# Kernel optimization log

Measured on AMD Instinct MI355X. Metric: run time of the kernel, lower is better.

## Reference

```python
import jax, jax.numpy as jnp
import numpy as np

N_SRC, N_DST, E = 32768, 8192, 65536
NODE_IN, EDGE_IN, HIDDEN = 64, 32, 64


def setup_inputs() -> dict:
    key = jax.random.key(0)
    ks = jax.random.split(key, 8)
    node_features = jax.random.normal(ks[0], (N_SRC, NODE_IN), dtype=jnp.float32)
    edge_features = jax.random.normal(ks[1], (E, EDGE_IN), dtype=jnp.float32)
    src_idx = jax.random.randint(ks[2], (E,), 0, N_SRC, dtype=jnp.int32)
    dst_idx = jax.random.randint(ks[3], (E,), 0, N_DST, dtype=jnp.int32)
    # edge_layer: Linear(edge_in, hidden*node_in); node_layer: Linear(node_in+hidden, hidden)
    s_e = 1.0 / np.sqrt(EDGE_IN)
    s_n = 1.0 / np.sqrt(NODE_IN + HIDDEN)
    W_e = jax.random.uniform(ks[4], (EDGE_IN, HIDDEN * NODE_IN), jnp.float32, -s_e, s_e)
    b_e = jax.random.uniform(ks[5], (HIDDEN * NODE_IN,), jnp.float32, -s_e, s_e)
    W_n = jax.random.uniform(ks[6], (NODE_IN + HIDDEN, HIDDEN), jnp.float32, -s_n, s_n)
    b_n = jax.random.uniform(ks[7], (HIDDEN,), jnp.float32, -s_n, s_n)
    return {"node_features": node_features, "edge_features": edge_features,
            "src_idx": src_idx, "dst_idx": dst_idx,
            "W_e": W_e, "b_e": b_e, "W_n": W_n, "b_n": b_n, "n_dst": N_DST}


def reference(node_features, edge_features, src_idx, dst_idx, W_e, b_e, W_n, b_n, n_dst):
    # Dropout is identity in eval mode.
    # Edge-conditioned weight generation: [E, hidden*node_in] -> [E, hidden, node_in]
    ew = jax.nn.relu(edge_features @ W_e + b_e).reshape(-1, HIDDEN, NODE_IN)
    h_src = node_features[src_idx]                       # [E, node_in] gather
    m = jnp.einsum('ehd,ed->eh', ew, h_src)              # per-edge matvec -> [E, hidden]
    # segment mean over destination nodes (mailbox mean)
    msum = jax.ops.segment_sum(m, dst_idx, num_segments=n_dst)
    cnt = jax.ops.segment_sum(jnp.ones((m.shape[0],), m.dtype), dst_idx, num_segments=n_dst)
    h_neigh = jnp.where(cnt[:, None] > 0, msum / jnp.maximum(cnt[:, None], 1.0), 0.0)
    h_self = node_features[:n_dst]
    h = jnp.concatenate([h_self, h_neigh], axis=1)       # [n_dst, node_in+hidden]
    return jax.nn.relu(h @ W_n + b_n)
```

## Files before the change

kernel.cpp:

```cpp
#include <hip/hip_runtime.h>


typedef float f32x4 __attribute__((ext_vector_type(4)));
typedef float f32x2 __attribute__((ext_vector_type(2)));
typedef __bf16 bf16x8 __attribute__((ext_vector_type(8)));
typedef __bf16 bf16x4 __attribute__((ext_vector_type(4)));

#define E_TOT   65536
#define NDST    8192
#define EPW     72
#define EPF     68

__global__ __launch_bounds__(256) void prep_kernel(
    const float* __restrict__ We, const float* __restrict__ be,
    __bf16* __restrict__ Wp, float* __restrict__ bp) {
  int tid = blockIdx.x * 256 + threadIdx.x;
  int T = tid >> 6, l = tid & 63;
  int d0 = T >> 2, ht = T & 3;
  int c = l & 15, kg = l >> 4;
  int ncol = (ht * 16 + c) * 64 + d0;
  bf16x8 v;
#pragma unroll
  for (int j = 0; j < 8; ++j) v[j] = (__bf16)We[(kg * 8 + j) * 4096 + ncol];
  *reinterpret_cast<bf16x8*>(Wp + tid * 8) = v;
  if (l < 16) bp[T * 16 + l] = be[(ht * 16 + l) * 64 + d0];
}

__global__ __launch_bounds__(256) void scan_kernel(const int* __restrict__ cnt_i,
                                                   int* __restrict__ off,
                                                   int* __restrict__ cursor) {
  __shared__ int wsum[4];
  const int t = threadIdx.x;
  const int lane = t & 63, w = t >> 6;
  int vals[32];
  const int4* cp = (const int4*)(cnt_i + t * 32);
#pragma unroll
  for (int i = 0; i < 8; ++i) {
    int4 v = cp[i];
    vals[i * 4 + 0] = v.x; vals[i * 4 + 1] = v.y;
    vals[i * 4 + 2] = v.z; vals[i * 4 + 3] = v.w;
  }
  int loc[32];
  int s = 0;
#pragma unroll
  for (int i = 0; i < 32; ++i) { loc[i] = s; s += vals[i]; }
  int inc = s;
#pragma unroll
  for (int d = 1; d < 64; d <<= 1) {
    int n = __shfl_up(inc, d, 64);
    if (lane >= d) inc += n;
  }
  if (lane == 63) wsum[w] = inc;
  __syncthreads();
  int base = inc - s;
#pragma unroll
  for (int i = 0; i < 4; ++i)
    if (i < w) base += wsum[i];
#pragma unroll
  for (int i = 0; i < 32; ++i) {
    int v = base + loc[i];
    off[t * 32 + i] = v;
    cursor[t * 32 + i] = v;
  }
  if (t == 255) off[8192] = E_TOT;
}

__global__ void fill_kernel(const int* __restrict__ dst, int* __restrict__ cursor,
                            int* __restrict__ eid) {
  int e = blockIdx.x * 256 + threadIdx.x;
  int slot = atomicAdd(&cursor[dst[e]], 1);
  eid[slot] = e;
}

__global__ __launch_bounds__(256, 2) void edge5_kernel(
    const float* __restrict__ nf, const float* __restrict__ ef,
    const int* __restrict__ src, const int* __restrict__ dst,
    const __bf16* __restrict__ Wp, const float* __restrict__ bp,
    float* __restrict__ m, int* __restrict__ cnt_i) {
  __shared__ float hs[64 * EPF];
  const int t = threadIdx.x;
  const int eblk = blockIdx.x << 6;

  {
    const int el = t & 63, q = t >> 6;
    const int srow = src[eblk + el];
    const f32x4* nfr = (const f32x4*)(nf + (srow << 6) + (q << 4));
#pragma unroll
    for (int i = 0; i < 4; ++i) {
      f32x4 v = nfr[i];
      const int dbase = (q << 4) + i * 4;
      hs[(dbase + 0) * EPF + el] = v[0];
      hs[(dbase + 1) * EPF + el] = v[1];
      hs[(dbase + 2) * EPF + el] = v[2];
      hs[(dbase + 3) * EPF + el] = v[3];
    }
  }

  if (t < 64) atomicAdd(&cnt_i[dst[eblk + t]], 1);

  const int w = t >> 6, l = t & 63;
  const int c = l & 15, g = l >> 4;

  bf16x8 afr[4];
#pragma unroll
  for (int as = 0; as < 4; ++as) {
    const int e = eblk + as * 16 + c;
    const f32x4* p = (const f32x4*)(ef + (e << 5) + (g << 3));
    f32x4 v0 = p[0], v1 = p[1];
    bf16x8 a;
    a[0] = (__bf16)v0[0]; a[1] = (__bf16)v0[1]; a[2] = (__bf16)v0[2]; a[3] = (__bf16)v0[3];
    a[4] = (__bf16)v1[0]; a[5] = (__bf16)v1[1]; a[6] = (__bf16)v1[2]; a[7] = (__bf16)v1[3];
    afr[as] = a;
  }

  __syncthreads();

  f32x2 accA[4], accB[4];
#pragma unroll
  for (int i = 0; i < 4; ++i) {
    accA[i][0] = 0.f; accA[i][1] = 0.f;
    accB[i][0] = 0.f; accB[i][1] = 0.f;
  }

  const bf16x8* WpV = (const bf16x8*)Wp;

  bf16x8 bfrA = WpV[(0 * 4 + w) * 64 + l];
  float  bvA  = bp[(0 * 4 + w) * 16 + c];
  bf16x8 bfrB = WpV[(1 * 4 + w) * 64 + l];
  float  bvB  = bp[(1 * 4 + w) * 16 + c];

#pragma unroll 8
  for (int dl = 0; dl < 64; dl += 2) {
    {
      const bf16x8 bcur = bfrA;
      const f32x4 cb = {bvA, bvA, bvA, bvA};
      if (dl + 2 < 64) {
        bfrA = WpV[((dl + 2) * 4 + w) * 64 + l];
        bvA  = bp[((dl + 2) * 4 + w) * 16 + c];
      }
#pragma unroll
      for (int as = 0; as < 4; ++as) {
        const f32x4 hvf = *(const f32x4*)&hs[dl * EPF + as * 16 + (g << 2)];
        f32x4 tmp = __builtin_amdgcn_mfma_f32_16x16x32_bf16(afr[as], bcur, cb, 0, 0, 0);
        f32x2 tl = {fmaxf(tmp[0], 0.f), fmaxf(tmp[1], 0.f)};
        f32x2 th = {fmaxf(tmp[2], 0.f), fmaxf(tmp[3], 0.f)};
        f32x2 hl = __builtin_shufflevector(hvf, hvf, 0, 1);
        f32x2 hh = __builtin_shufflevector(hvf, hvf, 2, 3);
        asm("v_pk_fma_f32 %0, %1, %2, %0" : "+v"(accA[as]) : "v"(tl), "v"(hl));
        asm("v_pk_fma_f32 %0, %1, %2, %0" : "+v"(accB[as]) : "v"(th), "v"(hh));
      }
    }
    {
      const bf16x8 bcur = bfrB;
      const f32x4 cb = {bvB, bvB, bvB, bvB};
      if (dl + 3 < 64) {
        bfrB = WpV[((dl + 3) * 4 + w) * 64 + l];
        bvB  = bp[((dl + 3) * 4 + w) * 16 + c];
      }
#pragma unroll
      for (int as = 0; as < 4; ++as) {
        const f32x4 hvf = *(const f32x4*)&hs[(dl + 1) * EPF + as * 16 + (g << 2)];
        f32x4 tmp = __builtin_amdgcn_mfma_f32_16x16x32_bf16(afr[as], bcur, cb, 0, 0, 0);
        f32x2 tl = {fmaxf(tmp[0], 0.f), fmaxf(tmp[1], 0.f)};
        f32x2 th = {fmaxf(tmp[2], 0.f), fmaxf(tmp[3], 0.f)};
        f32x2 hl = __builtin_shufflevector(hvf, hvf, 0, 1);
        f32x2 hh = __builtin_shufflevector(hvf, hvf, 2, 3);
        asm("v_pk_fma_f32 %0, %1, %2, %0" : "+v"(accA[as]) : "v"(tl), "v"(hl));
        asm("v_pk_fma_f32 %0, %1, %2, %0" : "+v"(accB[as]) : "v"(th), "v"(hh));
      }
    }
  }

  const int hbase = (w << 4) + c;
#pragma unroll
  for (int as = 0; as < 4; ++as) {
    const int ebase = eblk + as * 16 + (g << 2);
    m[((ebase + 0) << 6) + hbase] = accA[as][0];
    m[((ebase + 1) << 6) + hbase] = accA[as][1];
    m[((ebase + 2) << 6) + hbase] = accB[as][0];
    m[((ebase + 3) << 6) + hbase] = accB[as][1];
  }
}

__global__ __launch_bounds__(256) void final5_kernel(
    const float* __restrict__ nf, const float* __restrict__ m,
    const int* __restrict__ off, const int* __restrict__ eid,
    const float* __restrict__ Wn, const float* __restrict__ bn,
    float* __restrict__ out) {
  __shared__ float wn_s[128 * 64];
  __shared__ float hn_s[8 * 64];
  const int t = threadIdx.x;
#pragma unroll
  for (int i = 0; i < 8; ++i)
    ((f32x4*)wn_s)[i * 256 + t] = ((const f32x4*)Wn)[i * 256 + t];

  const int w = t >> 6, h = t & 63;
  const int row0 = blockIdx.x * 8 + w * 2;

#pragma unroll
  for (int i = 0; i < 2; ++i) {
    const int d = row0 + i;
    const int lo = off[d], hi = off[d + 1];
    float a0 = 0.f, a1 = 0.f;
    int j = lo;
    for (; j + 2 <= hi; j += 2) {
      const int e0 = eid[j], e1 = eid[j + 1];
      a0 += m[(e0 << 6) + h];
      a1 += m[(e1 << 6) + h];
    }
    if (j < hi) a0 += m[(eid[j] << 6) + h];
    const float a = a0 + a1;
    hn_s[(w * 2 + i) * 64 + h] = (hi > lo) ? a * (1.f / (float)(hi - lo)) : 0.f;
  }
  __syncthreads();

  const float bv = bn[h];
  float acc[2] = {bv, bv};
#pragma unroll 4
  for (int k = 0; k < 64; ++k) {
    const float wv = wn_s[k * 64 + h];
#pragma unroll
    for (int i = 0; i < 2; ++i)
      acc[i] = fmaf(nf[(row0 + i) * 64 + k], wv, acc[i]);
  }
#pragma unroll 4
  for (int k = 0; k < 64; ++k) {
    const float wv = wn_s[(64 + k) * 64 + h];
#pragma unroll
    for (int i = 0; i < 2; ++i)
      acc[i] = fmaf(hn_s[(w * 2 + i) * 64 + k], wv, acc[i]);
  }
#pragma unroll
  for (int i = 0; i < 2; ++i)
    out[(row0 + i) * 64 + h] = fmaxf(acc[i], 0.f);
}


__global__ __launch_bounds__(256, 4) void edge_kernel(
    const float* __restrict__ nf, const float* __restrict__ ef,
    const int* __restrict__ src, const int* __restrict__ dst,
    const __bf16* __restrict__ Wp, const float* __restrict__ bp,
    float* __restrict__ msum, float* __restrict__ cnt_g) {
  __shared__ __bf16 hs[64 * EPW];
  const int t = threadIdx.x;
  const int eblk = blockIdx.x << 6;
  {
    const int el = t & 63, q = t >> 6;
    const int srow = src[eblk + el];
    const f32x4* nfr = (const f32x4*)(nf + (srow << 6) + (q << 4));
#pragma unroll
    for (int i = 0; i < 4; ++i) {
      f32x4 v = nfr[i];
      const int dbase = (q << 4) + i * 4;
      hs[(dbase + 0) * EPW + el] = (__bf16)v[0];
      hs[(dbase + 1) * EPW + el] = (__bf16)v[1];
      hs[(dbase + 2) * EPW + el] = (__bf16)v[2];
      hs[(dbase + 3) * EPW + el] = (__bf16)v[3];
    }
  }
  const int w = t >> 6, l = t & 63, c = l & 15, g = l >> 4;
  bf16x8 afr[4];
#pragma unroll
  for (int as = 0; as < 4; ++as) {
    const int e = eblk + as * 16 + c;
    const f32x4* p = (const f32x4*)(ef + (e << 5) + (g << 3));
    f32x4 v0 = p[0], v1 = p[1];
    bf16x8 a;
    a[0] = (__bf16)v0[0]; a[1] = (__bf16)v0[1]; a[2] = (__bf16)v0[2]; a[3] = (__bf16)v0[3];
    a[4] = (__bf16)v1[0]; a[5] = (__bf16)v1[1]; a[6] = (__bf16)v1[2]; a[7] = (__bf16)v1[3];
    afr[as] = a;
  }
  __syncthreads();
  f32x4 acc[4];
#pragma unroll
  for (int i = 0; i < 4; ++i) { acc[i][0]=0.f; acc[i][1]=0.f; acc[i][2]=0.f; acc[i][3]=0.f; }
  const bf16x8* WpV = (const bf16x8*)Wp;
  const f32x4 zero = {0.f, 0.f, 0.f, 0.f};
#pragma unroll 4
  for (int d0 = 0; d0 < 64; ++d0) {
    const int T = d0 * 4 + w;
    const bf16x8 bfr = WpV[T * 64 + l];
    const float bv = bp[T * 16 + c];
    const f32x4 cb = {bv, bv, bv, bv};
#pragma unroll
    for (int as = 0; as < 4; ++as) {
      const bf16x4 hv = *(const bf16x4*)&hs[d0 * EPW + as * 16 + (g << 2)];
      const f32x4 hvf = {(float)hv[0], (float)hv[1], (float)hv[2], (float)hv[3]};
      f32x4 tmp = __builtin_amdgcn_mfma_f32_16x16x32_bf16(afr[as], bfr, cb, 0, 0, 0);
      tmp = __builtin_elementwise_max(tmp, zero);
      acc[as] = tmp * hvf + acc[as];
    }
  }
#pragma unroll
  for (int as = 0; as < 4; ++as)
#pragma unroll
    for (int r = 0; r < 4; ++r) {
      const int e = eblk + as * 16 + (g << 2) + r;
      const int dd = dst[e];
      unsafeAtomicAdd(msum + (dd << 6) + (w << 4) + c, acc[as][r]);
      if (w == 0 && c == 0) unsafeAtomicAdd(cnt_g + dd, 1.0f);
    }
}

__global__ __launch_bounds__(256) void final_kernel(
    const float* __restrict__ nf, const float* __restrict__ msum,
    const float* __restrict__ cnt, const float* __restrict__ Wn,
    const float* __restrict__ bn, float* __restrict__ out) {
  __shared__ float wn_s[128 * 64];
  const int t = threadIdx.x;
#pragma unroll
  for (int i = 0; i < 8; ++i)
    ((f32x4*)wn_s)[i * 256 + t] = ((const f32x4*)Wn)[i * 256 + t];
  __syncthreads();
  const int w = t >> 6, h = t & 63;
  const int row0 = blockIdx.x * 16 + w * 4;
  const float bv = bn[h];
  float acc[4] = {bv, bv, bv, bv};
  float s[4];
#pragma unroll
  for (int i = 0; i < 4; ++i) {
    const float cv = cnt[row0 + i];
    s[i] = cv > 0.f ? 1.f / cv : 0.f;
  }
#pragma unroll 4
  for (int k = 0; k < 64; ++k) {
    const float wv = wn_s[k * 64 + h];
#pragma unroll
    for (int i = 0; i < 4; ++i) acc[i] = fmaf(nf[(row0 + i) * 64 + k], wv, acc[i]);
  }
#pragma unroll 4
  for (int k = 0; k < 64; ++k) {
    const float wv = wn_s[(64 + k) * 64 + h];
#pragma unroll
    for (int i = 0; i < 4; ++i) acc[i] = fmaf(msum[(row0 + i) * 64 + k] * s[i], wv, acc[i]);
  }
#pragma unroll
  for (int i = 0; i < 4; ++i) out[(row0 + i) * 64 + h] = fmaxf(acc[i], 0.f);
}


extern "C" void kernel_launch(void* const* d_in, const int* in_sizes, int n_in,
                              void* d_out, int out_size, void* d_ws, size_t ws_size,
                              hipStream_t stream) {
  const float* nf  = (const float*)d_in[0];
  const float* ef  = (const float*)d_in[1];
  const int*   src = (const int*)d_in[2];
  const int*   dst = (const int*)d_in[3];
  const float* We  = (const float*)d_in[4];
  const float* be  = (const float*)d_in[5];
  const float* Wn  = (const float*)d_in[6];
  const float* bn  = (const float*)d_in[7];
  float* out = (float*)d_out;
  char* ws = (char*)d_ws;

  const size_t MB = 16777216;
  const size_t T_OFF    = MB;
  const size_t T_CURSOR = T_OFF + 36864;
  const size_t T_CNTI   = T_CURSOR + 32768;
  const size_t T_EID    = T_CNTI + 32768;
  const size_t T_WP     = T_EID + 262144;
  const size_t T_BP     = T_WP + 262144;
  const size_t NEED     = T_BP + 16384;

  if (ws_size >= NEED) {
    float*  m      = (float*)ws;
    int*    off    = (int*)(ws + T_OFF);
    int*    cursor = (int*)(ws + T_CURSOR);
    int*    cnt_i  = (int*)(ws + T_CNTI);
    int*    eid    = (int*)(ws + T_EID);
    __bf16* Wp     = (__bf16*)(ws + T_WP);
    float*  bp     = (float*)(ws + T_BP);

    hipMemsetAsync(cnt_i, 0, 32768, stream);
    prep_kernel<<<64, 256, 0, stream>>>(We, be, Wp, bp);
    edge5_kernel<<<E_TOT / 64, 256, 0, stream>>>(nf, ef, src, dst, Wp, bp, m, cnt_i);
    scan_kernel<<<1, 256, 0, stream>>>(cnt_i, off, cursor);
    fill_kernel<<<E_TOT / 256, 256, 0, stream>>>(dst, cursor, eid);
    final5_kernel<<<NDST / 8, 256, 0, stream>>>(nf, m, off, eid, Wn, bn, out);
  } else {
    float* msum = (float*)ws;
    float* cnt  = (float*)(ws + 2097152);
    const size_t need = 2097152 + 32768 + 262144 + 16384;
    __bf16* Wp;
    float*  bp;
    if (ws_size >= need) {
      Wp = (__bf16*)(ws + 2097152 + 32768);
      bp = (float*)(ws + 2097152 + 32768 + 262144);
    } else {
      Wp = (__bf16*)d_out;
      bp = (float*)((char*)d_out + 262144);
    }
    hipMemsetAsync(msum, 0, 2097152 + 32768, stream);
    prep_kernel<<<64, 256, 0, stream>>>(We, be, Wp, bp);
    edge_kernel<<<E_TOT / 64, 256, 0, stream>>>(nf, ef, src, dst, Wp, bp, msum, cnt);
    final_kernel<<<NDST / 16, 256, 0, stream>>>(nf, msum, cnt, Wn, bn, out);
  }
}
```

Measured before the change: 79.74 us.

## Remap edge kernel warps to edge subtiles sharing A fragment across hidden tiles

Each wave now owns 16 edges and loops over all four hidden tiles, instead of owning one hidden tile and looping over all 64 edges. It holds one A fragment (edge features) in registers but loads four B fragments per d step from global/L2, and reads one LDS vector per step instead of four. Launch bounds are raised to 4 blocks per SM to increase occupancy. The cost is four times as many weight-fragment loads per wave per step, and more live B registers under a tighter register budget.

```diff
diff --git a/kernel.cpp b/kernel.cpp
--- a/kernel.cpp
+++ b/kernel.cpp
@@ -72,7 +72,7 @@
   eid[slot] = e;
 }
 
-__global__ __launch_bounds__(256, 2) void edge5_kernel(
+__global__ __launch_bounds__(256, 4) void edge6_kernel(
     const float* __restrict__ nf, const float* __restrict__ ef,
     const int* __restrict__ src, const int* __restrict__ dst,
     const __bf16* __restrict__ Wp, const float* __restrict__ bp,
@@ -101,19 +101,33 @@
   const int w = t >> 6, l = t & 63;
   const int c = l & 15, g = l >> 4;
 
-  bf16x8 afr[4];
-#pragma unroll
-  for (int as = 0; as < 4; ++as) {
-    const int e = eblk + as * 16 + c;
+  bf16x8 afr;
+  {
+    const int e = eblk + (w << 4) + c;
     const f32x4* p = (const f32x4*)(ef + (e << 5) + (g << 3));
     f32x4 v0 = p[0], v1 = p[1];
-    bf16x8 a;
-    a[0] = (__bf16)v0[0]; a[1] = (__bf16)v0[1]; a[2] = (__bf16)v0[2]; a[3] = (__bf16)v0[3];
-    a[4] = (__bf16)v1[0]; a[5] = (__bf16)v1[1]; a[6] = (__bf16)v1[2]; a[7] = (__bf16)v1[3];
-    afr[as] = a;
-  }
-
-  __syncthreads();
+    afr[0] = (__bf16)v0[0]; afr[1] = (__bf16)v0[1]; afr[2] = (__bf16)v0[2]; afr[3] = (__bf16)v0[3];
+    afr[4] = (__bf16)v1[0]; afr[5] = (__bf16)v1[1]; afr[6] = (__bf16)v1[2]; afr[7] = (__bf16)v1[3];
+  }
+
+  const bf16x8* WpV = (const bf16x8*)Wp;
+
+  bf16x8 bA0 = WpV[(0 * 4 + 0) * 64 + l];
+  bf16x8 bA1 = WpV[(0 * 4 + 1) * 64 + l];
+  bf16x8 bA2 = WpV[(0 * 4 + 2) * 64 + l];
+  bf16x8 bA3 = WpV[(0 * 4 + 3) * 64 + l];
+  float  vA0 = bp[(0 * 4 + 0) * 16 + c];
+  float  vA1 = bp[(0 * 4 + 1) * 16 + c];
+  float  vA2 = bp[(0 * 4 + 2) * 16 + c];
+  float  vA3 = bp[(0 * 4 + 3) * 16 + c];
+  bf16x8 bB0 = WpV[(1 * 4 + 0) * 64 + l];
+  bf16x8 bB1 = WpV[(1 * 4 + 1) * 64 + l];
+  bf16x8 bB2 = WpV[(1 * 4 + 2) * 64 + l];
+  bf16x8 bB3 = WpV[(1 * 4 + 3) * 64 + l];
+  float  vB0 = bp[(1 * 4 + 0) * 16 + c];
+  float  vB1 = bp[(1 * 4 + 1) * 16 + c];
+  float  vB2 = bp[(1 * 4 + 2) * 16 + c];
+  float  vB3 = bp[(1 * 4 + 3) * 16 + c];
 
   f32x2 accA[4], accB[4];
 #pragma unroll
@@ -122,63 +136,84 @@
     accB[i][0] = 0.f; accB[i][1] = 0.f;
   }
 
-  const bf16x8* WpV = (const bf16x8*)Wp;
-
-  bf16x8 bfrA = WpV[(0 * 4 + w) * 64 + l];
-  float  bvA  = bp[(0 * 4 + w) * 16 + c];
-  bf16x8 bfrB = WpV[(1 * 4 + w) * 64 + l];
-  float  bvB  = bp[(1 * 4 + w) * 16 + c];
-
-#pragma unroll 8
-  for (int dl = 0; dl < 64; dl += 2) {
+  __syncthreads();
+
+  const int hoff = (w << 4) + (g << 2);
+  f32x4 hvA = *(const f32x4*)&hs[0 * EPF + hoff];
+  f32x4 hvB = *(const f32x4*)&hs[1 * EPF + hoff];
+
+#define EDGE_SECTION(B0, B1, B2, B3, V0, V1, V2, V3, HV)                            \
+  {                                                                                  \
+    const f32x4 cb0 = {V0, V0, V0, V0};                                              \
+    const f32x4 cb1 = {V1, V1, V1, V1};                                              \
+    const f32x4 cb2 = {V2, V2, V2, V2};                                              \
+    const f32x4 cb3 = {V3, V3, V3, V3};                                              \
+    f32x4 t0 = __builtin_amdgcn_mfma_f32_16x16x32_bf16(afr, B0, cb0, 0, 0, 0);       \
+    f32x4 t1 = __builtin_amdgcn_mfma_f32_16x16x32_bf16(afr, B1, cb1, 0, 0, 0);       \
+    f32x4 t2 = __builtin_amdgcn_mfma_f32_16x16x32_bf16(afr, B2, cb2, 0, 0, 0);       \
+    f32x4 t3 = __builtin_amdgcn_mfma_f32_16x16x32_bf16(afr, B3, cb3, 0, 0, 0);       \
+    f32x2 hl = __builtin_shufflevector(HV, HV, 0, 1);                                \
+    f32x2 hh = __builtin_shufflevector(HV, HV, 2, 3);                                \
+    f32x2 p;                                                                         \
+    p[0] = fmaxf(t0[0], 0.f); p[1] = fmaxf(t0[1], 0.f);                              \
+    asm("v_pk_fma_f32 %0, %1, %2, %0" : "+v"(accA[0]) : "v"(p), "v"(hl));            \
+    p[0] = fmaxf(t0[2], 0.f); p[1] = fmaxf(t0[3], 0.f);                              \
+    asm("v_pk_fma_f32 %0, %1, %2, %0" : "+v"(accB[0]) : "v"(p), "v"(hh));            \
+    p[0] = fmaxf(t1[0], 0.f); p[1] = fmaxf(t1[1], 0.f);                              \
+    asm("v_pk_fma_f32 %0, %1, %2, %0" : "+v"(accA[1]) : "v"(p), "v"(hl));            \
+    p[0] = fmaxf(t1[2], 0.f); p[1] = fmaxf(t1[3], 0.f);                              \
+    asm("v_pk_fma_f32 %0, %1, %2, %0" : "+v"(accB[1]) : "v"(p), "v"(hh));            \
+    p[0] = fmaxf(t2[0], 0.f); p[1] = fmaxf(t2[1], 0.f);                              \
+    asm("v_pk_fma_f32 %0, %1, %2, %0" : "+v"(accA[2]) : "v"(p), "v"(hl));            \
+    p[0] = fmaxf(t2[2], 0.f); p[1] = fmaxf(t2[3], 0.f);                              \
+    asm("v_pk_fma_f32 %0, %1, %2, %0" : "+v"(accB[2]) : "v"(p), "v"(hh));            \
+    p[0] = fmaxf(t3[0], 0.f); p[1] = fmaxf(t3[1], 0.f);                              \
+    asm("v_pk_fma_f32 %0, %1, %2, %0" : "+v"(accA[3]) : "v"(p), "v"(hl));            \
+    p[0] = fmaxf(t3[2], 0.f); p[1] = fmaxf(t3[3], 0.f);                              \
+    asm("v_pk_fma_f32 %0, %1, %2, %0" : "+v"(accB[3]) : "v"(p), "v"(hh));            \
+  }
+
+  for (int d0 = 0; d0 < 64; d0 += 2) {
     {
-      const bf16x8 bcur = bfrA;
-      const f32x4 cb = {bvA, bvA, bvA, bvA};
-      if (dl + 2 < 64) {
-        bfrA = WpV[((dl + 2) * 4 + w) * 64 + l];
-        bvA  = bp[((dl + 2) * 4 + w) * 16 + c];
+      const bf16x8 u0 = bA0, u1 = bA1, u2 = bA2, u3 = bA3;
+      const float  x0 = vA0, x1 = vA1, x2 = vA2, x3 = vA3;
+      const f32x4  hv = hvA;
+      if (d0 + 2 < 64) {
+        const int Tn = (d0 + 2) * 4;
+        bA0 = WpV[(Tn + 0) * 64 + l];  vA0 = bp[(Tn + 0) * 16 + c];
+        bA1 = WpV[(Tn + 1) * 64 + l];  vA1 = bp[(Tn + 1) * 16 + c];
+        bA2 = WpV[(Tn + 2) * 64 + l];  vA2 = bp[(Tn + 2) * 16 + c];
+        bA3 = WpV[(Tn + 3) * 64 + l];  vA3 = bp[(Tn + 3) * 16 + c];
+        hvA = *(const f32x4*)&hs[(d0 + 2) * EPF + hoff];
       }
-#pragma unroll
-      for (int as = 0; as < 4; ++as) {
-        const f32x4 hvf = *(const f32x4*)&hs[dl * EPF + as * 16 + (g << 2)];
-        f32x4 tmp = __builtin_amdgcn_mfma_f32_16x16x32_bf16(afr[as], bcur, cb, 0, 0, 0);
-        f32x2 tl = {fmaxf(tmp[0], 0.f), fmaxf(tmp[1], 0.f)};
-        f32x2 th = {fmaxf(tmp[2], 0.f), fmaxf(tmp[3], 0.f)};
-        f32x2 hl = __builtin_shufflevector(hvf, hvf, 0, 1);
-        f32x2 hh = __builtin_shufflevector(hvf, hvf, 2, 3);
-        asm("v_pk_fma_f32 %0, %1, %2, %0" : "+v"(accA[as]) : "v"(tl), "v"(hl));
-        asm("v_pk_fma_f32 %0, %1, %2, %0" : "+v"(accB[as]) : "v"(th), "v"(hh));
+      EDGE_SECTION(u0, u1, u2, u3, x0, x1, x2, x3, hv)
+    }
+    {
+      const bf16x8 u0 = bB0, u1 = bB1, u2 = bB2, u3 = bB3;
+      const float  x0 = vB0, x1 = vB1, x2 = vB2, x3 = vB3;
+      const f32x4  hv = hvB;
+      if (d0 + 3 < 64) {
+        const int Tn = (d0 + 3) * 4;
+        bB0 = WpV[(Tn + 0) * 64 + l];  vB0 = bp[(Tn + 0) * 16 + c];
+        bB1 = WpV[(Tn + 1) * 64 + l];  vB1 = bp[(Tn + 1) * 16 + c];
+        bB2 = WpV[(Tn + 2) * 64 + l];  vB2 = bp[(Tn + 2) * 16 + c];
+        bB3 = WpV[(Tn + 3) * 64 + l];  vB3 = bp[(Tn + 3) * 16 + c];
+        hvB = *(const f32x4*)&hs[(d0 + 3) * EPF + hoff];
       }
-    }
-    {
-      const bf16x8 bcur = bfrB;
-      const f32x4 cb = {bvB, bvB, bvB, bvB};
-      if (dl + 3 < 64) {
-        bfrB = WpV[((dl + 3) * 4 + w) * 64 + l];
-        bvB  = bp[((dl + 3) * 4 + w) * 16 + c];
-      }
-#pragma unroll
-      for (int as = 0; as < 4; ++as) {
-        const f32x4 hvf = *(const f32x4*)&hs[(dl + 1) * EPF + as * 16 + (g << 2)];
-        f32x4 tmp = __builtin_amdgcn_mfma_f32_16x16x32_bf16(afr[as], bcur, cb, 0, 0, 0);
-        f32x2 tl = {fmaxf(tmp[0], 0.f), fmaxf(tmp[1], 0.f)};
-        f32x2 th = {fmaxf(tmp[2], 0.f), fmaxf(tmp[3], 0.f)};
-        f32x2 hl = __builtin_shufflevector(hvf, hvf, 0, 1);
-        f32x2 hh = __builtin_shufflevector(hvf, hvf, 2, 3);
-        asm("v_pk_fma_f32 %0, %1, %2, %0" : "+v"(accA[as]) : "v"(tl), "v"(hl));
-        asm("v_pk_fma_f32 %0, %1, %2, %0" : "+v"(accB[as]) : "v"(th), "v"(hh));
-      }
-    }
-  }
-
-  const int hbase = (w << 4) + c;
-#pragma unroll
-  for (int as = 0; as < 4; ++as) {
-    const int ebase = eblk + as * 16 + (g << 2);
-    m[((ebase + 0) << 6) + hbase] = accA[as][0];
-    m[((ebase + 1) << 6) + hbase] = accA[as][1];
-    m[((ebase + 2) << 6) + hbase] = accB[as][0];
-    m[((ebase + 3) << 6) + hbase] = accB[as][1];
+      EDGE_SECTION(u0, u1, u2, u3, x0, x1, x2, x3, hv)
+    }
+  }
+#undef EDGE_SECTION
+
+  const int ebase = eblk + (w << 4) + (g << 2);
+#pragma unroll
+  for (int ht = 0; ht < 4; ++ht) {
+    const int hcol = (ht << 4) + c;
+    f32x2 a = accA[ht], b = accB[ht];
+    m[((ebase + 0) << 6) + hcol] = a[0];
+    m[((ebase + 1) << 6) + hcol] = a[1];
+    m[((ebase + 2) << 6) + hcol] = b[0];
+    m[((ebase + 3) << 6) + hcol] = b[1];
   }
 }
 
@@ -373,7 +408,7 @@
 
     hipMemsetAsync(cnt_i, 0, 32768, stream);
     prep_kernel<<<64, 256, 0, stream>>>(We, be, Wp, bp);
-    edge5_kernel<<<E_TOT / 64, 256, 0, stream>>>(nf, ef, src, dst, Wp, bp, m, cnt_i);
+    edge6_kernel<<<E_TOT / 64, 256, 0, stream>>>(nf, ef, src, dst, Wp, bp, m, cnt_i);
     scan_kernel<<<1, 256, 0, stream>>>(cnt_i, off, cursor);
     fill_kernel<<<E_TOT / 256, 256, 0, stream>>>(dst, cursor, eid);
     final5_kernel<<<NDST / 8, 256, 0, stream>>>(nf, m, off, eid, Wn, bn, out);
```

After: 117.6 us. 47.5% more time.

## Restructure edge kernel: 128 edges per block, double-buffered LDS weight staging

Applied to the files above, without the earlier changes.

The edge kernel now handles 128 edges per block instead of 64. Each wave owns 32 edges across all 64 hidden columns, and the generated-weight fragments are staged through double-buffered shared memory in 16 windows. This raises reuse of the W_e fragments loaded from global memory and halves the block count. Gathered source-node features are stored in LDS as bf16, which shrinks LDS traffic but adds rounding error. The separate memset of the degree counter is folded into the prep kernel, saving one launch.

```diff
diff --git a/kernel.cpp b/kernel.cpp
--- a/kernel.cpp
+++ b/kernel.cpp
@@ -9,12 +9,13 @@
 #define E_TOT   65536
 #define NDST    8192
 #define EPW     72
-#define EPF     68
+#define EP2     136
 
 __global__ __launch_bounds__(256) void prep_kernel(
     const float* __restrict__ We, const float* __restrict__ be,
-    __bf16* __restrict__ Wp, float* __restrict__ bp) {
+    __bf16* __restrict__ Wp, float* __restrict__ bp, int* __restrict__ cnt_i) {
   int tid = blockIdx.x * 256 + threadIdx.x;
+  if (tid < NDST) cnt_i[tid] = 0;
   int T = tid >> 6, l = tid & 63;
   int d0 = T >> 2, ht = T & 3;
   int c = l & 15, kg = l >> 4;
@@ -72,113 +73,132 @@
   eid[slot] = e;
 }
 
-__global__ __launch_bounds__(256, 2) void edge5_kernel(
+__global__ __launch_bounds__(256, 2) void edge7_kernel(
     const float* __restrict__ nf, const float* __restrict__ ef,
     const int* __restrict__ src, const int* __restrict__ dst,
     const __bf16* __restrict__ Wp, const float* __restrict__ bp,
     float* __restrict__ m, int* __restrict__ cnt_i) {
-  __shared__ float hs[64 * EPF];
+  __shared__ __align__(16) __bf16 hs[64 * EP2];
+  __shared__ uint4 wp_s[2][1024];
+  __shared__ float bias_s[2][256];
   const int t = threadIdx.x;
-  const int eblk = blockIdx.x << 6;
+  const int eblk = blockIdx.x << 7;
 
   {
-    const int el = t & 63, q = t >> 6;
+    const int el = t & 127, q = t >> 7;
     const int srow = src[eblk + el];
-    const f32x4* nfr = (const f32x4*)(nf + (srow << 6) + (q << 4));
-#pragma unroll
-    for (int i = 0; i < 4; ++i) {
+    const f32x4* nfr = (const f32x4*)(nf + (srow << 6) + (q << 5));
+#pragma unroll
+    for (int i = 0; i < 8; ++i) {
       f32x4 v = nfr[i];
-      const int dbase = (q << 4) + i * 4;
-      hs[(dbase + 0) * EPF + el] = v[0];
-      hs[(dbase + 1) * EPF + el] = v[1];
-      hs[(dbase + 2) * EPF + el] = v[2];
-      hs[(dbase + 3) * EPF + el] = v[3];
-    }
-  }
-
-  if (t < 64) atomicAdd(&cnt_i[dst[eblk + t]], 1);
+      const int d = (q << 5) + (i << 2);
+      hs[(d + 0) * EP2 + el] = (__bf16)v[0];
+      hs[(d + 1) * EP2 + el] = (__bf16)v[1];
+      hs[(d + 2) * EP2 + el] = (__bf16)v[2];
+      hs[(d + 3) * EP2 + el] = (__bf16)v[3];
+    }
+  }
+
+  if (t < 128) atomicAdd(&cnt_i[dst[eblk + t]], 1);
 
   const int w = t >> 6, l = t & 63;
   const int c = l & 15, g = l >> 4;
-
-  bf16x8 afr[4];
-#pragma unroll
-  for (int as = 0; as < 4; ++as) {
-    const int e = eblk + as * 16 + c;
-    const f32x4* p = (const f32x4*)(ef + (e << 5) + (g << 3));
-    f32x4 v0 = p[0], v1 = p[1];
-    bf16x8 a;
-    a[0] = (__bf16)v0[0]; a[1] = (__bf16)v0[1]; a[2] = (__bf16)v0[2]; a[3] = (__bf16)v0[3];
-    a[4] = (__bf16)v1[0]; a[5] = (__bf16)v1[1]; a[6] = (__bf16)v1[2]; a[7] = (__bf16)v1[3];
-    afr[as] = a;
+  const uint4* WpQ = (const uint4*)Wp;
+  const int bpos = (((t >> 6) * 16) + (t & 15)) * 4 + ((t >> 4) & 3);
+
+  bf16x8 afrA, afrB;
+  {
+    const int e0 = eblk + (w << 5) + c;
+    const f32x4* p0 = (const f32x4*)(ef + (e0 << 5) + (g << 3));
+    f32x4 v0 = p0[0], v1 = p0[1];
+    afrA[0] = (__bf16)v0[0]; afrA[1] = (__bf16)v0[1]; afrA[2] = (__bf16)v0[2]; afrA[3] = (__bf16)v0[3];
+    afrA[4] = (__bf16)v1[0]; afrA[5] = (__bf16)v1[1]; afrA[6] = (__bf16)v1[2]; afrA[7] = (__bf16)v1[3];
+    const f32x4* p1 = (const f32x4*)(ef + ((e0 + 16) << 5) + (g << 3));
+    f32x4 u0 = p1[0], u1 = p1[1];
+    afrB[0] = (__bf16)u0[0]; afrB[1] = (__bf16)u0[1]; afrB[2] = (__bf16)u0[2]; afrB[3] = (__bf16)u0[3];
+    afrB[4] = (__bf16)u1[0]; afrB[5] = (__bf16)u1[1]; afrB[6] = (__bf16)u1[2]; afrB[7] = (__bf16)u1[3];
+  }
+
+  {
+    uint4 s0 = WpQ[t], s1 = WpQ[256 + t], s2 = WpQ[512 + t], s3 = WpQ[768 + t];
+    float sb = bp[t];
+    wp_s[0][t] = s0; wp_s[0][256 + t] = s1; wp_s[0][512 + t] = s2; wp_s[0][768 + t] = s3;
+    bias_s[0][bpos] = sb;
+  }
+
+  f32x4 accA[4], accB[4];
+#pragma unroll
+  for (int i = 0; i < 4; ++i) {
+    accA[i][0]=0.f; accA[i][1]=0.f; accA[i][2]=0.f; accA[i][3]=0.f;
+    accB[i][0]=0.f; accB[i][1]=0.f; accB[i][2]=0.f; accB[i][3]=0.f;
   }
 
   __syncthreads();
 
-  f32x2 accA[4], accB[4];
-#pragma unroll
-  for (int i = 0; i < 4; ++i) {
-    accA[i][0] = 0.f; accA[i][1] = 0.f;
-    accB[i][0] = 0.f; accB[i][1] = 0.f;
-  }
-
-  const bf16x8* WpV = (const bf16x8*)Wp;
-
-  bf16x8 bfrA = WpV[(0 * 4 + w) * 64 + l];
-  float  bvA  = bp[(0 * 4 + w) * 16 + c];
-  bf16x8 bfrB = WpV[(1 * 4 + w) * 64 + l];
-  float  bvB  = bp[(1 * 4 + w) * 16 + c];
-
-#pragma unroll 8
-  for (int dl = 0; dl < 64; dl += 2) {
-    {
-      const bf16x8 bcur = bfrA;
-      const f32x4 cb = {bvA, bvA, bvA, bvA};
-      if (dl + 2 < 64) {
-        bfrA = WpV[((dl + 2) * 4 + w) * 64 + l];
-        bvA  = bp[((dl + 2) * 4 + w) * 16 + c];
+  const int hoffA = (w << 5) + (g << 2);
+  int cur = 0;
+
+  for (int win = 0; win < 16; ++win) {
+    uint4 s0, s1, s2, s3; float sb;
+    const bool pf = (win < 15);
+    if (pf) {
+      const int base = (win + 1) << 10;
+      s0 = WpQ[base + t]; s1 = WpQ[base + 256 + t];
+      s2 = WpQ[base + 512 + t]; s3 = WpQ[base + 768 + t];
+      sb = bp[((win + 1) << 8) + t];
+    }
+
+    const bf16x8* wpf = (const bf16x8*)&wp_s[cur][0];
+    const float*  bsf = &bias_s[cur][0];
+#pragma unroll
+    for (int dl = 0; dl < 4; ++dl) {
+      const int d0 = (win << 2) + dl;
+      const bf16x8 wf0 = wpf[(dl * 4 + 0) * 64 + l];
+      const bf16x8 wf1 = wpf[(dl * 4 + 1) * 64 + l];
+      const bf16x8 wf2 = wpf[(dl * 4 + 2) * 64 + l];
+      const bf16x8 wf3 = wpf[(dl * 4 + 3) * 64 + l];
+      const f32x4  bv4 = *(const f32x4*)&bsf[(dl * 16 + c) * 4];
+      const bf16x4 hva = *(const bf16x4*)&hs[d0 * EP2 + hoffA];
+      const bf16x4 hvb = *(const bf16x4*)&hs[d0 * EP2 + hoffA + 16];
+      const f32x4 ha = {(float)hva[0], (float)hva[1], (float)hva[2], (float)hva[3]};
+      const f32x4 hb = {(float)hvb[0], (float)hvb[1], (float)hvb[2], (float)hvb[3]};
+      const f32x4 zero = {0.f, 0.f, 0.f, 0.f};
+#define DO_HT(HT, WF)                                                                 \
+      {                                                                               \
+        const f32x4 cb = {bv4[HT], bv4[HT], bv4[HT], bv4[HT]};                        \
+        f32x4 ta = __builtin_amdgcn_mfma_f32_16x16x32_bf16(afrA, WF, cb, 0, 0, 0);    \
+        ta = __builtin_elementwise_max(ta, zero);                                     \
+        accA[HT] = ta * ha + accA[HT];                                                \
+        f32x4 tb = __builtin_amdgcn_mfma_f32_16x16x32_bf16(afrB, WF, cb, 0, 0, 0);    \
+        tb = __builtin_elementwise_max(tb, zero);                                     \
+        accB[HT] = tb * hb + accB[HT];                                                \
       }
-#pragma unroll
-      for (int as = 0; as < 4; ++as) {
-        const f32x4 hvf = *(const f32x4*)&hs[dl * EPF + as * 16 + (g << 2)];
-        f32x4 tmp = __builtin_amdgcn_mfma_f32_16x16x32_bf16(afr[as], bcur, cb, 0, 0, 0);
-        f32x2 tl = {fmaxf(tmp[0], 0.f), fmaxf(tmp[1], 0.f)};
-        f32x2 th = {fmaxf(tmp[2], 0.f), fmaxf(tmp[3], 0.f)};
-        f32x2 hl = __builtin_shufflevector(hvf, hvf, 0, 1);
-        f32x2 hh = __builtin_shufflevector(hvf, hvf, 2, 3);
-        asm("v_pk_fma_f32 %0, %1, %2, %0" : "+v"(accA[as]) : "v"(tl), "v"(hl));
-        asm("v_pk_fma_f32 %0, %1, %2, %0" : "+v"(accB[as]) : "v"(th), "v"(hh));
-      }
-    }
-    {
-      const bf16x8 bcur = bfrB;
-      const f32x4 cb = {bvB, bvB, bvB, bvB};
-      if (dl + 3 < 64) {
-        bfrB = WpV[((dl + 3) * 4 + w) * 64 + l];
-        bvB  = bp[((dl + 3) * 4 + w) * 16 + c];
-      }
-#pragma unroll
-      for (int as = 0; as < 4; ++as) {
-        const f32x4 hvf = *(const f32x4*)&hs[(dl + 1) * EPF + as * 16 + (g << 2)];
-        f32x4 tmp = __builtin_amdgcn_mfma_f32_16x16x32_bf16(afr[as], bcur, cb, 0, 0, 0);
-        f32x2 tl = {fmaxf(tmp[0], 0.f), fmaxf(tmp[1], 0.f)};
-        f32x2 th = {fmaxf(tmp[2], 0.f), fmaxf(tmp[3], 0.f)};
-        f32x2 hl = __builtin_shufflevector(hvf, hvf, 0, 1);
-        f32x2 hh = __builtin_shufflevector(hvf, hvf, 2, 3);
-        asm("v_pk_fma_f32 %0, %1, %2, %0" : "+v"(accA[as]) : "v"(tl), "v"(hl));
-        asm("v_pk_fma_f32 %0, %1, %2, %0" : "+v"(accB[as]) : "v"(th), "v"(hh));
-      }
-    }
-  }
-
-  const int hbase = (w << 4) + c;
-#pragma unroll
-  for (int as = 0; as < 4; ++as) {
-    const int ebase = eblk + as * 16 + (g << 2);
-    m[((ebase + 0) << 6) + hbase] = accA[as][0];
-    m[((ebase + 1) << 6) + hbase] = accA[as][1];
-    m[((ebase + 2) << 6) + hbase] = accB[as][0];
-    m[((ebase + 3) << 6) + hbase] = accB[as][1];
+      DO_HT(0, wf0) DO_HT(1, wf1) DO_HT(2, wf2) DO_HT(3, wf3)
+#undef DO_HT
+    }
+
+    if (pf) {
+      const int nb = cur ^ 1;
+      wp_s[nb][t] = s0; wp_s[nb][256 + t] = s1;
+      wp_s[nb][512 + t] = s2; wp_s[nb][768 + t] = s3;
+      bias_s[nb][bpos] = sb;
+    }
+    __syncthreads();
+    cur ^= 1;
+  }
+
+  const int e0 = eblk + (w << 5) + (g << 2);
+#pragma unroll
+  for (int ht = 0; ht < 4; ++ht) {
+    const int col = (ht << 4) + c;
+    m[((e0 + 0) << 6) + col] = accA[ht][0];
+    m[((e0 + 1) << 6) + col] = accA[ht][1];
+    m[((e0 + 2) << 6) + col] = accA[ht][2];
+    m[((e0 + 3) << 6) + col] = accA[ht][3];
+    m[((e0 + 16) << 6) + col] = accB[ht][0];
+    m[((e0 + 17) << 6) + col] = accB[ht][1];
+    m[((e0 + 18) << 6) + col] = accB[ht][2];
+    m[((e0 + 19) << 6) + col] = accB[ht][3];
   }
 }
 
@@ -371,9 +391,8 @@
     __bf16* Wp     = (__bf16*)(ws + T_WP);
     float*  bp     = (float*)(ws + T_BP);
 
-    hipMemsetAsync(cnt_i, 0, 32768, stream);
-    prep_kernel<<<64, 256, 0, stream>>>(We, be, Wp, bp);
-    edge5_kernel<<<E_TOT / 64, 256, 0, stream>>>(nf, ef, src, dst, Wp, bp, m, cnt_i);
+    prep_kernel<<<64, 256, 0, stream>>>(We, be, Wp, bp, cnt_i);
+    edge7_kernel<<<E_TOT / 128, 256, 0, stream>>>(nf, ef, src, dst, Wp, bp, m, cnt_i);
     scan_kernel<<<1, 256, 0, stream>>>(cnt_i, off, cursor);
     fill_kernel<<<E_TOT / 256, 256, 0, stream>>>(dst, cursor, eid);
     final5_kernel<<<NDST / 8, 256, 0, stream>>>(nf, m, off, eid, Wn, bn, out);
@@ -391,7 +410,7 @@
       bp = (float*)((char*)d_out + 262144);
     }
     hipMemsetAsync(msum, 0, 2097152 + 32768, stream);
-    prep_kernel<<<64, 256, 0, stream>>>(We, be, Wp, bp);
+    prep_kernel<<<64, 256, 0, stream>>>(We, be, Wp, bp, (int*)cnt);
     edge_kernel<<<E_TOT / 64, 256, 0, stream>>>(nf, ef, src, dst, Wp, bp, msum, cnt);
     final_kernel<<<NDST / 16, 256, 0, stream>>>(nf, msum, cnt, Wn, bn, out);
   }
```

Result: slower. 104.0 us (+30.4%).

## Stage edge weight tiles through LDS windows and fold counter zeroing into prep

Applied to the files above, without the earlier changes.

The edge kernel now loads the packed bf16 edge-layer weights and biases into shared memory in eight windows of 8 input dims, using global_load_lds when it is available. Before, each wave streamed its weight fragments from global memory with register prefetch. This is meant to cut repeated global/L2 traffic per MFMA step. In exchange it adds 32KB+ of LDS per block, which may reduce occupancy, plus two barriers per window with no overlap between loading and compute. Separately, the cnt_i memset is folded into prep_kernel to remove one launch.

```diff
diff --git a/kernel.cpp b/kernel.cpp
--- a/kernel.cpp
+++ b/kernel.cpp
@@ -11,10 +11,17 @@
 #define EPW     72
 #define EPF     68
 
+#if defined(__has_builtin)
+#if __has_builtin(__builtin_amdgcn_global_load_lds)
+#define HAVE_GLL 1
+#endif
+#endif
+
 __global__ __launch_bounds__(256) void prep_kernel(
     const float* __restrict__ We, const float* __restrict__ be,
-    __bf16* __restrict__ Wp, float* __restrict__ bp) {
+    __bf16* __restrict__ Wp, float* __restrict__ bp, int* __restrict__ cnt_i) {
   int tid = blockIdx.x * 256 + threadIdx.x;
+  if (tid < NDST) cnt_i[tid] = 0;
   int T = tid >> 6, l = tid & 63;
   int d0 = T >> 2, ht = T & 3;
   int c = l & 15, kg = l >> 4;
@@ -72,12 +79,14 @@
   eid[slot] = e;
 }
 
-__global__ __launch_bounds__(256, 2) void edge5_kernel(
+__global__ __launch_bounds__(256, 2) void edge8_kernel(
     const float* __restrict__ nf, const float* __restrict__ ef,
     const int* __restrict__ src, const int* __restrict__ dst,
     const __bf16* __restrict__ Wp, const float* __restrict__ bp,
     float* __restrict__ m, int* __restrict__ cnt_i) {
-  __shared__ float hs[64 * EPF];
+  __shared__ __align__(16) float hs[64 * EPF];
+  __shared__ __align__(16) __bf16 wwin[16384];
+  __shared__ __align__(16) float bwin[512];
   const int t = threadIdx.x;
   const int eblk = blockIdx.x << 6;
 
@@ -113,8 +122,6 @@
     afr[as] = a;
   }
 
-  __syncthreads();
-
   f32x2 accA[4], accB[4];
 #pragma unroll
   for (int i = 0; i < 4; ++i) {
@@ -122,26 +129,42 @@
     accB[i][0] = 0.f; accB[i][1] = 0.f;
   }
 
-  const bf16x8* WpV = (const bf16x8*)Wp;
-
-  bf16x8 bfrA = WpV[(0 * 4 + w) * 64 + l];
-  float  bvA  = bp[(0 * 4 + w) * 16 + c];
-  bf16x8 bfrB = WpV[(1 * 4 + w) * 64 + l];
-  float  bvB  = bp[(1 * 4 + w) * 16 + c];
-
-#pragma unroll 8
-  for (int dl = 0; dl < 64; dl += 2) {
+  const bf16x8* wv = (const bf16x8*)wwin;
+
+  for (int win = 0; win < 8; ++win) {
+#ifdef HAVE_GLL
     {
-      const bf16x8 bcur = bfrA;
-      const f32x4 cb = {bvA, bvA, bvA, bvA};
-      if (dl + 2 < 64) {
-        bfrA = WpV[((dl + 2) * 4 + w) * 64 + l];
-        bvA  = bp[((dl + 2) * 4 + w) * 16 + c];
+      const char* gbase = (const char*)Wp + ((size_t)win << 15) + ((size_t)w << 13) + ((size_t)l << 4);
+      char* lbase = (char*)wwin + (w << 13);
+#pragma unroll
+      for (int it = 0; it < 8; ++it) {
+        auto gp = (const __attribute__((address_space(1))) uint32_t*)(uintptr_t)(gbase + (it << 10));
+        auto lp = (__attribute__((address_space(3))) uint32_t*)(uintptr_t)(lbase + (it << 10));
+        __builtin_amdgcn_global_load_lds(gp, lp, 16, 0, 0);
       }
+    }
+#else
+    {
+      const uint4* gq = (const uint4*)((const char*)Wp + ((size_t)win << 15));
+      uint4* lq = (uint4*)wwin;
+#pragma unroll
+      for (int it = 0; it < 8; ++it) lq[t + (it << 8)] = gq[t + (it << 8)];
+    }
+#endif
+    bwin[t] = bp[(win << 9) + t];
+    bwin[t + 256] = bp[(win << 9) + 256 + t];
+    __syncthreads();
+
+#pragma unroll
+    for (int dl = 0; dl < 8; ++dl) {
+      const int d0 = (win << 3) + dl;
+      const bf16x8 bfr = wv[(dl * 4 + w) * 64 + l];
+      const float bv = bwin[(dl * 4 + w) * 16 + c];
+      const f32x4 cb = {bv, bv, bv, bv};
 #pragma unroll
       for (int as = 0; as < 4; ++as) {
-        const f32x4 hvf = *(const f32x4*)&hs[dl * EPF + as * 16 + (g << 2)];
-        f32x4 tmp = __builtin_amdgcn_mfma_f32_16x16x32_bf16(afr[as], bcur, cb, 0, 0, 0);
+        const f32x4 hvf = *(const f32x4*)&hs[d0 * EPF + as * 16 + (g << 2)];
+        f32x4 tmp = __builtin_amdgcn_mfma_f32_16x16x32_bf16(afr[as], bfr, cb, 0, 0, 0);
         f32x2 tl = {fmaxf(tmp[0], 0.f), fmaxf(tmp[1], 0.f)};
         f32x2 th = {fmaxf(tmp[2], 0.f), fmaxf(tmp[3], 0.f)};
         f32x2 hl = __builtin_shufflevector(hvf, hvf, 0, 1);
@@ -150,25 +173,7 @@
         asm("v_pk_fma_f32 %0, %1, %2, %0" : "+v"(accB[as]) : "v"(th), "v"(hh));
       }
     }
-    {
-      const bf16x8 bcur = bfrB;
-      const f32x4 cb = {bvB, bvB, bvB, bvB};
-      if (dl + 3 < 64) {
-        bfrB = WpV[((dl + 3) * 4 + w) * 64 + l];
-        bvB  = bp[((dl + 3) * 4 + w) * 16 + c];
-      }
-#pragma unroll
-      for (int as = 0; as < 4; ++as) {
-        const f32x4 hvf = *(const f32x4*)&hs[(dl + 1) * EPF + as * 16 + (g << 2)];
-        f32x4 tmp = __builtin_amdgcn_mfma_f32_16x16x32_bf16(afr[as], bcur, cb, 0, 0, 0);
-        f32x2 tl = {fmaxf(tmp[0], 0.f), fmaxf(tmp[1], 0.f)};
-        f32x2 th = {fmaxf(tmp[2], 0.f), fmaxf(tmp[3], 0.f)};
-        f32x2 hl = __builtin_shufflevector(hvf, hvf, 0, 1);
-        f32x2 hh = __builtin_shufflevector(hvf, hvf, 2, 3);
-        asm("v_pk_fma_f32 %0, %1, %2, %0" : "+v"(accA[as]) : "v"(tl), "v"(hl));
-        asm("v_pk_fma_f32 %0, %1, %2, %0" : "+v"(accB[as]) : "v"(th), "v"(hh));
-      }
-    }
+    __syncthreads();
   }
 
   const int hbase = (w << 4) + c;
@@ -371,9 +376,8 @@
     __bf16* Wp     = (__bf16*)(ws + T_WP);
     float*  bp     = (float*)(ws + T_BP);
 
-    hipMemsetAsync(cnt_i, 0, 32768, stream);
-    prep_kernel<<<64, 256, 0, stream>>>(We, be, Wp, bp);
-    edge5_kernel<<<E_TOT / 64, 256, 0, stream>>>(nf, ef, src, dst, Wp, bp, m, cnt_i);
+    prep_kernel<<<64, 256, 0, stream>>>(We, be, Wp, bp, cnt_i);
+    edge8_kernel<<<E_TOT / 64, 256, 0, stream>>>(nf, ef, src, dst, Wp, bp, m, cnt_i);
     scan_kernel<<<1, 256, 0, stream>>>(cnt_i, off, cursor);
     fill_kernel<<<E_TOT / 256, 256, 0, stream>>>(dst, cursor, eid);
     final5_kernel<<<NDST / 8, 256, 0, stream>>>(nf, m, off, eid, Wn, bn, out);
@@ -391,7 +395,7 @@
       bp = (float*)((char*)d_out + 262144);
     }
     hipMemsetAsync(msum, 0, 2097152 + 32768, stream);
-    prep_kernel<<<64, 256, 0, stream>>>(We, be, Wp, bp);
+    prep_kernel<<<64, 256, 0, stream>>>(We, be, Wp, bp, (int*)cnt);
     edge_kernel<<<E_TOT / 64, 256, 0, stream>>>(nf, ef, src, dst, Wp, bp, msum, cnt);
     final_kernel<<<NDST / 16, 256, 0, stream>>>(nf, msum, cnt, Wn, bn, out);
   }
```

Result: slower. 81.82 us (+2.6%).
